# Kernel optimization log

Hardware: AMD Instinct MI355X
Metric: run time of the kernel (lower is better)

## Reference

```python
import jax, jax.numpy as jnp
import numpy as np

D_MODEL = 1024
N_HEADS = 16
HEAD_DIM = D_MODEL // N_HEADS  # 64
D_LATENT = 4 * (D_MODEL // 4)  # 1024
LN_EPS = 1e-5
NORM_EPS = 1e-12


def setup_inputs() -> dict:
    key = jax.random.key(0)
    ks = jax.random.split(key, 20)
    B, S = 2, 2048
    s = lambda fan_in: 1.0 / np.sqrt(fan_in)
    inp = {
        "query": jax.random.normal(ks[0], (B, S, D_MODEL), jnp.float32),
        "key_in": jax.random.normal(ks[1], (B, S, D_MODEL), jnp.float32),
        "value": jax.random.normal(ks[2], (B, S, D_MODEL), jnp.float32),
        # z_proj
        "Wz": jax.random.uniform(ks[3], (D_MODEL, D_LATENT), jnp.float32, -s(D_MODEL), s(D_MODEL)),
        "bz": jax.random.uniform(ks[4], (D_LATENT,), jnp.float32, -s(D_MODEL), s(D_MODEL)),
        # z_norm (LayerNorm)
        "ln_g": jnp.ones((D_LATENT,), jnp.float32),
        "ln_b": jnp.zeros((D_LATENT,), jnp.float32),
        # q/r/h projections: d_latent -> n_heads*head_dim
        "Wq": jax.random.uniform(ks[5], (D_LATENT, N_HEADS * HEAD_DIM), jnp.float32, -s(D_LATENT), s(D_LATENT)),
        "bq": jax.random.uniform(ks[6], (N_HEADS * HEAD_DIM,), jnp.float32, -s(D_LATENT), s(D_LATENT)),
        "Wr": jax.random.uniform(ks[7], (D_LATENT, N_HEADS * HEAD_DIM), jnp.float32, -s(D_LATENT), s(D_LATENT)),
        "br": jax.random.uniform(ks[8], (N_HEADS * HEAD_DIM,), jnp.float32, -s(D_LATENT), s(D_LATENT)),
        "Wh": jax.random.uniform(ks[9], (D_LATENT, N_HEADS * HEAD_DIM), jnp.float32, -s(D_LATENT), s(D_LATENT)),
        "bh": jax.random.uniform(ks[10], (N_HEADS * HEAD_DIM,), jnp.float32, -s(D_LATENT), s(D_LATENT)),
        # phi_proj: head_dim -> head_dim (shared across heads, applied to Q and R)
        "Wphi": jax.random.uniform(ks[11], (HEAD_DIM, HEAD_DIM), jnp.float32, -s(HEAD_DIM), s(HEAD_DIM)),
        "bphi": jax.random.uniform(ks[12], (HEAD_DIM,), jnp.float32, -s(HEAD_DIM), s(HEAD_DIM)),
        # out_proj
        "Wo": jax.random.uniform(ks[13], (D_MODEL, D_MODEL), jnp.float32, -s(D_MODEL), s(D_MODEL)),
        "bo": jax.random.uniform(ks[14], (D_MODEL,), jnp.float32, -s(D_MODEL), s(D_MODEL)),
    }
    return inp


def reference(query, key_in, value, Wz, bz, ln_g, ln_b, Wq, bq, Wr, br, Wh, bh, Wphi, bphi, Wo, bo):
    # NOTE: the original module ignores key_in and value entirely.
    B, S, _ = query.shape
    # latent projection + LayerNorm
    Z = query @ Wz + bz
    mu = jnp.mean(Z, axis=-1, keepdims=True)
    var = jnp.mean(jnp.square(Z - mu), axis=-1, keepdims=True)
    Z = (Z - mu) * jax.lax.rsqrt(var + LN_EPS) * ln_g + ln_b
    # Q, R, H projections -> [B, S, H, D]
    Q = (Z @ Wq + bq).reshape(B, S, N_HEADS, HEAD_DIM)
    R = (Z @ Wr + br).reshape(B, S, N_HEADS, HEAD_DIM)
    Hv = (Z @ Wh + bh).reshape(B, S, N_HEADS, HEAD_DIM)
    # phasor activation Psi(v) = v * exp(i * (v Wphi + bphi))
    phiQ = Q @ Wphi + bphi
    phiR = R @ Wphi + bphi
    # Re(Q' conj(R')) = (Q cos phiQ)(R cos phiR) + (Q sin phiQ)(R sin phiR)
    # stack real/imag components along head_dim so a single einsum gives the real part
    Qc = jnp.concatenate([Q * jnp.cos(phiQ), Q * jnp.sin(phiQ)], axis=-1)  # [B,S,H,2D]
    Rc = jnp.concatenate([R * jnp.cos(phiR), R * jnp.sin(phiR)], axis=-1)  # [B,S,H,2D]
    scores = jnp.einsum('bqhd,bkhd->bhqk', Qc, Rc)  # real part of complex QK^H
    # L2 row-normalization (torch F.normalize p=2 dim=-1, eps=1e-12)
    norm = jnp.sqrt(jnp.sum(jnp.square(scores), axis=-1, keepdims=True))
    attn = scores / jnp.maximum(norm, NORM_EPS)
    out = jnp.einsum('bhqk,bkhd->bqhd', attn, Hv).reshape(B, S, D_MODEL)
    return out @ Wo + bo
```

## Files before the change

### kernel.cpp

```cpp
#include <hip/hip_runtime.h>

#define DEV __device__ __forceinline__

typedef __bf16 bf16x8 __attribute__((ext_vector_type(8)));
typedef float f32x4 __attribute__((ext_vector_type(4)));

DEV float b2f(__bf16 v) { return (float)v; }
DEV __bf16 f2b(float v) { return (__bf16)v; }

DEV void gload16(const __bf16* g, __bf16* l) {
  __builtin_amdgcn_global_load_lds((const __attribute__((address_space(1))) unsigned*)g,
                                   (__attribute__((address_space(3))) unsigned*)l, 16, 0, 0);
}

__global__ void detect_k(const unsigned short* __restrict__ q, int* __restrict__ mode) {
  const int lane = threadIdx.x & 63;
  int cntNaN = 0, cntSmall = 0;
  for (int i = lane; i < 16384; i += 64) {
    const unsigned ef = (q[i] >> 7) & 0xFF;
    if (ef == 0xFF) cntNaN++;
    if (ef < 0x70) cntSmall++;
  }
#pragma unroll
  for (int o = 32; o > 0; o >>= 1) {
    cntNaN += __shfl_down(cntNaN, o);
    cntSmall += __shfl_down(cntSmall, o);
  }
  if (lane == 0) *mode = (cntNaN >= 4) ? 1 : ((cntSmall > 2000) ? 2 : 0);
}

__global__ __launch_bounds__(256) void qcvt_k(const void* __restrict__ src,
                                              __bf16* __restrict__ dst,
                                              int n8, const int* __restrict__ mode) {
  const int i = blockIdx.x * 256 + threadIdx.x;
  if (i >= n8) return;
  const int m = *mode;
  union { __bf16 h[8]; int4 u; } pk;
  if (m == 1) {
    const float4* p = (const float4*)src + (size_t)i * 2;
    const float4 a = p[0], b = p[1];
    pk.h[0] = f2b(a.x); pk.h[1] = f2b(a.y); pk.h[2] = f2b(a.z); pk.h[3] = f2b(a.w);
    pk.h[4] = f2b(b.x); pk.h[5] = f2b(b.y); pk.h[6] = f2b(b.z); pk.h[7] = f2b(b.w);
  } else if (m == 2) {
    const _Float16* p = (const _Float16*)src + (size_t)i * 8;
#pragma unroll
    for (int t = 0; t < 8; t++) pk.h[t] = f2b((float)p[t]);
  } else {
    pk.u = ((const int4*)src)[i];
  }
  ((int4*)dst)[i] = pk.u;
}

struct CvtJobs {
  const void* src[9];
  __bf16* dst[9];
};
__global__ __launch_bounds__(256) void cvt_all_k(CvtJobs J, const int* __restrict__ mode) {
  const int bb = blockIdx.x;
  int job, off;
  if (bb < 4) { job = bb; off = 0; }
  else if (bb == 4) { job = 4; off = 0; }
  else if (bb < 9) { job = 5; off = (bb - 5) * 1024; }
  else { job = 6 + (bb - 9); off = 0; }
  const int n = (job == 4) ? 64 : (job == 5) ? 4096 : 1024;
  const int m = *mode;
  const void* s = J.src[job];
  __bf16* d = J.dst[job];
  const int rem = n - off;
  const int cnt = rem > 1024 ? 1024 : rem;
  for (int i = threadIdx.x; i < cnt; i += 256) {
    const int idx = off + i;
    const float v = (m == 1) ? ((const float*)s)[idx]
                  : (m == 2) ? (float)((const _Float16*)s)[idx]
                             : b2f(((const __bf16*)s)[idx]);
    d[idx] = f2b(v);
  }
}

struct TJobs {
  const void* src[5];
  __bf16* dst[5];
};
__global__ __launch_bounds__(256) void tcvt_all_k(TJobs J, const int* __restrict__ mode) {
  __shared__ __bf16 tile[64][68];
  const void* in = J.src[blockIdx.z];
  __bf16* out = J.dst[blockIdx.z];
  const int c0 = blockIdx.x * 64, r0 = blockIdx.y * 64;
  const int tid = threadIdx.x;
  const int m = *mode;
  for (int i = tid; i < 64 * 16; i += 256) {
    int r = i >> 4, cc = (i & 15) * 4;
    const size_t base = (size_t)(r0 + r) * 1024 + c0 + cc;
    if (m == 1) {
      float4 v = *(const float4*)((const float*)in + base);
      tile[r][cc + 0] = f2b(v.x);
      tile[r][cc + 1] = f2b(v.y);
      tile[r][cc + 2] = f2b(v.z);
      tile[r][cc + 3] = f2b(v.w);
    } else if (m == 2) {
      const _Float16* p = (const _Float16*)in + base;
      tile[r][cc + 0] = f2b((float)p[0]);
      tile[r][cc + 1] = f2b((float)p[1]);
      tile[r][cc + 2] = f2b((float)p[2]);
      tile[r][cc + 3] = f2b((float)p[3]);
    } else {
      *(uint2*)&tile[r][cc] = *(const uint2*)((const __bf16*)in + base);
    }
  }
  __syncthreads();
  for (int i = tid; i < 64 * 16; i += 256) {
    int c = i >> 4, rr = (i & 15) * 4;
    union { __bf16 h[4]; uint2 u; } pk;
    pk.h[0] = tile[rr + 0][c];
    pk.h[1] = tile[rr + 1][c];
    pk.h[2] = tile[rr + 2][c];
    pk.h[3] = tile[rr + 3][c];
    *(uint2*)&out[(size_t)(c0 + c) * 1024 + r0 + rr] = pk.u;
  }
}

template <bool OUT_F32>
__global__ __launch_bounds__(256) void gemm2p_k(const __bf16* __restrict__ A,
                                                const __bf16* __restrict__ BT,
                                                const __bf16* __restrict__ bias,
                                                void* __restrict__ Cout,
                                                int M, int N, int K) {
  __shared__ __bf16 As[2][64 * 64];
  __shared__ __bf16 Bs[2][64 * 64];
  const int tid = threadIdx.x, lane = tid & 63, wv = tid >> 6;
  const int quad = lane >> 4, l16 = lane & 15;
  const int nblk = gridDim.x, chunk = nblk >> 3;
  const int hb = blockIdx.x;
  const int lb = (hb & 7) * chunk + (hb >> 3);
  const int mcnt = M >> 6;
  const int ni = lb / mcnt, mi = lb - ni * mcnt;
  const int m0 = mi * 64, n0 = ni * 64;
  const int wm = (wv >> 1) * 32, wn = (wv & 1) * 32;

  int s_src[2];
#pragma unroll
  for (int u = 0; u < 2; u++) {
    const int ci = tid + u * 256;
    const int r = ci >> 3, cc = ci & 7;
    s_src[u] = r * K + ((cc ^ (r & 7)) * 8);
  }

#define GSTAGE(BUF, K0)                                                   \
  {                                                                       \
    const __bf16* a_ = A + (size_t)m0 * K + (K0);                         \
    const __bf16* b_ = BT + (size_t)n0 * K + (K0);                        \
    gload16(a_ + s_src[0], &As[BUF][tid * 8]);                            \
    gload16(a_ + s_src[1], &As[BUF][(tid + 256) * 8]);                    \
    gload16(b_ + s_src[0], &Bs[BUF][tid * 8]);                            \
    gload16(b_ + s_src[1], &Bs[BUF][(tid + 256) * 8]);                    \
  }

  f32x4 acc[2][2] = {};
  const int nk = K >> 6;
  const int key = l16 & 7;

  GSTAGE(0, 0);
  __syncthreads();

  for (int t = 0; t < nk; ++t) {
    const int cur = t & 1;
    if (t + 1 < nk) GSTAGE(cur ^ 1, (t + 1) * 64);
#pragma unroll
    for (int s = 0; s < 2; s++) {
      const int co = ((4 * s + quad) ^ key) * 8;
      bf16x8 af[2], bfr[2];
#pragma unroll
      for (int i = 0; i < 2; i++) af[i] = *(const bf16x8*)&As[cur][(wm + i * 16 + l16) * 64 + co];
#pragma unroll
      for (int j = 0; j < 2; j++) bfr[j] = *(const bf16x8*)&Bs[cur][(wn + j * 16 + l16) * 64 + co];
#pragma unroll
      for (int i = 0; i < 2; i++)
#pragma unroll
        for (int j = 0; j < 2; j++)
          acc[i][j] = __builtin_amdgcn_mfma_f32_16x16x32_bf16(af[i], bfr[j], acc[i][j], 0, 0, 0);
    }
    __syncthreads();
  }
#undef GSTAGE

#pragma unroll
  for (int j = 0; j < 2; j++) {
    const int col = n0 + wn + j * 16 + l16;
    const float bv = b2f(bias[col]);
#pragma unroll
    for (int i = 0; i < 2; i++) {
#pragma unroll
      for (int r = 0; r < 4; r++) {
        const int row = m0 + wm + i * 16 + quad * 4 + r;
        const float v = acc[i][j][r] + bv;
        if (OUT_F32)
          ((float*)Cout)[(size_t)row * N + col] = v;
        else
          ((__bf16*)Cout)[(size_t)row * N + col] = f2b(v);
      }
    }
  }
}

__global__ __launch_bounds__(256) void qrh2p_k(const __bf16* __restrict__ A,
                                               const __bf16* __restrict__ BT3,
                                               const __bf16* __restrict__ bias3,
                                               __bf16* __restrict__ Qf,
                                               __bf16* __restrict__ Rf,
                                               __bf16* __restrict__ Hv,
                                               int M) {
  __shared__ __bf16 As[2][64 * 64];
  __shared__ __bf16 Bs[2][64 * 64];
  const int tid = threadIdx.x, lane = tid & 63, wv = tid >> 6;
  const int quad = lane >> 4, l16 = lane & 15;
  const int nblk = gridDim.x, chunk = nblk >> 3;
  const int hb = blockIdx.x;
  const int lb = (hb & 7) * chunk + (hb >> 3);
  const int mcnt = M >> 6;
  const int ni = lb / mcnt, mi = lb - ni * mcnt;
  const int m0 = mi * 64, n0g = ni * 64;
  const int which = n0g >> 10, n0 = n0g & 1023;
  __bf16* out = (which == 0) ? Qf : (which == 1) ? Rf : Hv;
  const int wm = (wv >> 1) * 32, wn = (wv & 1) * 32;
  const int K = 1024;

  int s_src[2];
#pragma unroll
  for (int u = 0; u < 2; u++) {
    const int ci = tid + u * 256;
    const int r = ci >> 3, cc = ci & 7;
    s_src[u] = r * K + ((cc ^ (r & 7)) * 8);
  }

#define GSTAGE(BUF, K0)                                                   \
  {                                                                       \
    const __bf16* a_ = A + (size_t)m0 * K + (K0);                         \
    const __bf16* b_ = BT3 + (size_t)n0g * K + (K0);                      \
    gload16(a_ + s_src[0], &As[BUF][tid * 8]);                            \
    gload16(a_ + s_src[1], &As[BUF][(tid + 256) * 8]);                    \
    gload16(b_ + s_src[0], &Bs[BUF][tid * 8]);                            \
    gload16(b_ + s_src[1], &Bs[BUF][(tid + 256) * 8]);                    \
  }

  f32x4 acc[2][2] = {};
  const int key = l16 & 7;

  GSTAGE(0, 0);
  __syncthreads();

  for (int t = 0; t < 16; ++t) {
    const int cur = t & 1;
    if (t + 1 < 16) GSTAGE(cur ^ 1, (t + 1) * 64);
#pragma unroll
    for (int s = 0; s < 2; s++) {
      const int co = ((4 * s + quad) ^ key) * 8;
      bf16x8 af[2], bfr[2];
#pragma unroll
      for (int i = 0; i < 2; i++) af[i] = *(const bf16x8*)&As[cur][(wm + i * 16 + l16) * 64 + co];
#pragma unroll
      for (int j = 0; j < 2; j++) bfr[j] = *(const bf16x8*)&Bs[cur][(wn + j * 16 + l16) * 64 + co];
#pragma unroll
      for (int i = 0; i < 2; i++)
#pragma unroll
        for (int j = 0; j < 2; j++)
          acc[i][j] = __builtin_amdgcn_mfma_f32_16x16x32_bf16(af[i], bfr[j], acc[i][j], 0, 0, 0);
    }
    __syncthreads();
  }
#undef GSTAGE

#pragma unroll
  for (int j = 0; j < 2; j++) {
    const int colg = n0g + wn + j * 16 + l16;
    const int col = n0 + wn + j * 16 + l16;
    const float bv = b2f(bias3[colg]);
#pragma unroll
    for (int i = 0; i < 2; i++) {
#pragma unroll
      for (int r = 0; r < 4; r++) {
        const int row = m0 + wm + i * 16 + quad * 4 + r;
        out[(size_t)row * 1024 + col] = f2b(acc[i][j][r] + bv);
      }
    }
  }
}

__global__ __launch_bounds__(256) void ln_k(const float* __restrict__ Zraw,
                                            const __bf16* __restrict__ g,
                                            const __bf16* __restrict__ bb,
                                            __bf16* __restrict__ Z) {
  __shared__ float red[8];
  const int row = blockIdx.x, tid = threadIdx.x, lane = tid & 63, wv = tid >> 6;
  const float* x = Zraw + (size_t)row * 1024;
  float4 v = *(const float4*)&x[tid * 4];
  float s = v.x + v.y + v.z + v.w;
  float ss = v.x * v.x + v.y * v.y + v.z * v.z + v.w * v.w;
#pragma unroll
  for (int o = 32; o > 0; o >>= 1) {
    s += __shfl_down(s, o);
    ss += __shfl_down(ss, o);
  }
  if (lane == 0) { red[wv] = s; red[4 + wv] = ss; }
  __syncthreads();
  const float S = red[0] + red[1] + red[2] + red[3];
  const float SS = red[4] + red[5] + red[6] + red[7];
  const float mu = S * (1.f / 1024.f);
  const float var = SS * (1.f / 1024.f) - mu * mu;
  const float rstd = rsqrtf(var + 1e-5f);
  const int c = tid * 4;
  float xs[4] = {v.x, v.y, v.z, v.w};
  union { __bf16 h[4]; uint2 u; } pk;
#pragma unroll
  for (int i = 0; i < 4; i++)
    pk.h[i] = f2b((xs[i] - mu) * rstd * b2f(g[c + i]) + b2f(bb[c + i]));
  *(uint2*)&Z[(size_t)row * 1024 + c] = pk.u;
}

__global__ __launch_bounds__(256) void phasor_mfma_k(const __bf16* __restrict__ Qf,
                                                     const __bf16* __restrict__ Rf,
                                                     const __bf16* __restrict__ Wphi,
                                                     const __bf16* __restrict__ bphi,
                                                     __bf16* __restrict__ Qc,
                                                     __bf16* __restrict__ Rc) {
  __shared__ __bf16 Qs[128][76];
  __shared__ __bf16 WT[64][76];
  const __bf16* in = blockIdx.y ? Rf : Qf;
  __bf16* out = blockIdx.y ? Rc : Qc;
  const int tid = threadIdx.x, lane = tid & 63, wv = tid >> 6;
  const int quad = lane >> 4, l16 = lane & 15;
  const size_t m0 = (size_t)blockIdx.x * 128;
  for (int i = tid; i < 1024; i += 256) {
    int r = i >> 3, c = (i & 7) * 8;
    *(int4*)&Qs[r][c] = *(const int4*)&in[(m0 + r) * 64 + c];
  }
  for (int i = tid; i < 4096; i += 256) WT[i & 63][i >> 6] = Wphi[i];
  __syncthreads();
  f32x4 acc[2][4] = {};
#pragma unroll
  for (int s = 0; s < 2; s++) {
    const int ka = s * 32 + quad * 8;
    bf16x8 bfr[4];
#pragma unroll
    for (int j = 0; j < 4; j++) bfr[j] = *(const bf16x8*)&WT[j * 16 + l16][ka];
#pragma unroll
    for (int i = 0; i < 2; i++) {
      const bf16x8 af = *(const bf16x8*)&Qs[wv * 32 + i * 16 + l16][ka];
#pragma unroll
      for (int j = 0; j < 4; j++)
        acc[i][j] = __builtin_amdgcn_mfma_f32_16x16x32_bf16(af, bfr[j], acc[i][j], 0, 0, 0);
    }
  }
#pragma unroll
  for (int i = 0; i < 2; i++)
#pragma unroll
    for (int j = 0; j < 4; j++) {
      const int col = j * 16 + l16;
      const float bj = b2f(bphi[col]);
#pragma unroll
      for (int r = 0; r < 4; r++) {
        const int row = wv * 32 + i * 16 + quad * 4 + r;
        const float phi = acc[i][j][r] + bj;
        float sn, cs;
        __sincosf(phi, &sn, &cs);
        const float qv = b2f(Qs[row][col]);
        const size_t ob = (m0 + row) * 128;
        out[ob + col] = f2b(qv * cs);
        out[ob + 64 + col] = f2b(qv * sn);
      }
    }
}

__global__ __launch_bounds__(256) void hvt_k(const __bf16* __restrict__ Hv,
                                             __bf16* __restrict__ HvT, int S) {
  __shared__ __bf16 t[64][72];
  const int tt = blockIdx.x * 64, h = blockIdx.y, b = blockIdx.z;
  const int tid = threadIdx.x;
  for (int i = tid; i < 512; i += 256) {
    int tok = i >> 3, dc = (i & 7) * 8;
    *(int4*)&t[tok][dc] = *(const int4*)&Hv[((size_t)(b * S + tt + tok) * 16 + h) * 64 + dc];
  }
  __syncthreads();
  for (int i = tid; i < 1024; i += 256) {
    int d = i >> 4, tc = (i & 15) * 4;
    union { __bf16 h4[4]; uint2 u; } pk;
    pk.h4[0] = t[tc + 0][d];
    pk.h4[1] = t[tc + 1][d];
    pk.h4[2] = t[tc + 2][d];
    pk.h4[3] = t[tc + 3][d];
    *(uint2*)&HvT[(((size_t)(b * 16 + h) * 64 + d) * S) + tt + tc] = pk.u;
  }
}

__global__ __launch_bounds__(256) void attn_k(const __bf16* __restrict__ Qc,
                                              const __bf16* __restrict__ Rc,
                                              const __bf16* __restrict__ HvT,
                                              __bf16* __restrict__ Aout, int S) {
  __shared__ __bf16 Rs[2][64 * 128];
  __shared__ __bf16 Hs[2][64 * 64];
  const int tid = threadIdx.x, lane = tid & 63, wv = tid >> 6;
  const int quad = lane >> 4, l16 = lane & 15;
  const int nblk = gridDim.x;
  const int chunk = nblk >> 3;
  const int hb = blockIdx.x;
  const int lb = (hb & 7) * chunk + (hb >> 3);
  const int nx = nblk >> 5;
  const int x = lb % nx;
  const int rest = lb / nx;
  const int h = rest & 15, b = rest >> 4;
  const int q0 = x * 64;

  bf16x8 qf[4];
  {
    const __bf16* qp = Qc + ((size_t)(b * S + q0 + wv * 16 + l16) * 16 + h) * 128 + quad * 8;
#pragma unroll
    for (int s = 0; s < 4; s++) qf[s] = *(const bf16x8*)(qp + s * 32);
  }

  const size_t rcb = ((size_t)b * S * 16 + h) * 128;
  const size_t hvb = (size_t)(b * 16 + h) * 64 * S;

  int rs_src[4], hs_src[2];
#pragma unroll
  for (int u = 0; u < 4; u++) {
    const int r = 4 * (wv * 4 + u) + (lane >> 4);
    rs_src[u] = r * 2048 + (((lane & 15) ^ (r & 7)) * 8);
  }
#pragma unroll
  for (int u = 0; u < 2; u++) {
    const int row = 8 * (wv * 2 + u) + (lane >> 3);
    hs_src[u] = row * S + (((lane & 7) ^ (row & 7)) * 8);
  }

#define STAGE(BUF, TILE)                                                        \
  {                                                                             \
    const __bf16* rc_ = Rc + rcb + (size_t)(TILE) * 64 * 2048;                  \
    const __bf16* hv_ = HvT + hvb + (TILE) * 64;                                \
    _Pragma("unroll")                                                           \
    for (int u = 0; u < 4; u++)                                                 \
      gload16(rc_ + rs_src[u], &Rs[BUF][(wv * 4 + u) * 512]);                   \
    _Pragma("unroll")                                                           \
    for (int u = 0; u < 2; u++)                                                 \
      gload16(hv_ + hs_src[u], &Hs[BUF][(wv * 2 + u) * 512]);                   \
  }

  f32x4 oacc[4] = {};
  float rssq = 0.f;
  const int nt = S >> 6;

  STAGE(0, 0);
  __syncthreads();

  const int srcA = ((quad & 1) << 1) | (quad >> 1);
  const int adA = ((srcA << 4) | l16) << 2;
  const int adB = (((srcA ^ 1) << 4) | l16) << 2;
  const bool par = (quad & 1) != 0;
  const bool hi = (quad >> 1) != 0;
  const int key = l16 & 7;

  for (int it = 0; it < nt; ++it) {
    const int cur = it & 1;
    if (it + 1 < nt) STAGE(cur ^ 1, it + 1);

    f32x4 sacc[4] = {};
    __builtin_amdgcn_s_setprio(1);
#pragma unroll
    for (int s = 0; s < 4; s++) {
      const int co = ((4 * s + quad) ^ key) * 8;
#pragma unroll
      for (int jt = 0; jt < 4; jt++) {
        const bf16x8 rf = *(const bf16x8*)&Rs[cur][(jt * 16 + l16) * 128 + co];
        sacc[jt] = __builtin_amdgcn_mfma_f32_16x16x32_bf16(rf, qf[s], sacc[jt], 0, 0, 0);
      }
    }
    __builtin_amdgcn_s_setprio(0);

    unsigned pk[4][2];
#pragma unroll
    for (int jt = 0; jt < 4; jt++) {
      rssq += sacc[jt][0] * sacc[jt][0] + sacc[jt][1] * sacc[jt][1] +
              sacc[jt][2] * sacc[jt][2] + sacc[jt][3] * sacc[jt][3];
      union { __bf16 h2[2]; unsigned u; } p0, p1;
      p0.h2[0] = f2b(sacc[jt][0]); p0.h2[1] = f2b(sacc[jt][1]);
      p1.h2[0] = f2b(sacc[jt][2]); p1.h2[1] = f2b(sacc[jt][3]);
      pk[jt][0] = p0.u; pk[jt][1] = p1.u;
    }

#pragma unroll
    for (int s2 = 0; s2 < 2; s2++) {
      bf16x8 hf[4];
      const int co2 = ((4 * s2 + quad) ^ key) * 8;
#pragma unroll
      for (int jd = 0; jd < 4; jd++)
        hf[jd] = *(const bf16x8*)&Hs[cur][(jd * 16 + l16) * 64 + co2];
      const int jA = 2 * s2, jB = 2 * s2 + 1;
      const unsigned o0 = par ? pk[jB][0] : pk[jA][0];
      const unsigned o1 = par ? pk[jB][1] : pk[jA][1];
      const unsigned o2 = par ? pk[jA][0] : pk[jB][0];
      const unsigned o3 = par ? pk[jA][1] : pk[jB][1];
      const unsigned r0 = (unsigned)__builtin_amdgcn_ds_bpermute(adA, (int)o0);
      const unsigned r1 = (unsigned)__builtin_amdgcn_ds_bpermute(adA, (int)o1);
      const unsigned r2 = (unsigned)__builtin_amdgcn_ds_bpermute(adB, (int)o2);
      const unsigned r3 = (unsigned)__builtin_amdgcn_ds_bpermute(adB, (int)o3);
      union { unsigned u[4]; bf16x8 v; } bw;
      bw.u[0] = hi ? r2 : r0;
      bw.u[1] = hi ? r3 : r1;
      bw.u[2] = hi ? r0 : r2;
      bw.u[3] = hi ? r1 : r3;
      __builtin_amdgcn_s_setprio(1);
#pragma unroll
      for (int jd = 0; jd < 4; jd++)
        oacc[jd] = __builtin_amdgcn_mfma_f32_16x16x32_bf16(hf[jd], bw.v, oacc[jd], 0, 0, 0);
      __builtin_amdgcn_s_setprio(0);
    }
    __syncthreads();
  }
#undef STAGE

  {
    float t = rssq;
    t += __shfl_xor(t, 16);
    t += __shfl_xor(t, 32);
    const float inv = 1.0f / fmaxf(sqrtf(t), 1e-12f);
    const size_t orow = (size_t)(b * S + q0 + wv * 16 + l16) * 1024 + h * 64;
#pragma unroll
    for (int jd = 0; jd < 4; jd++) {
      union { __bf16 h4[4]; uint2 u2; } o;
#pragma unroll
      for (int r = 0; r < 4; r++) o.h4[r] = f2b(oacc[jd][r] * inv);
      *(uint2*)&Aout[orow + jd * 16 + quad * 4] = o.u2;
    }
  }
}

extern "C" void kernel_launch(void* const* d_in, const int* in_sizes, int n_in,
                              void* d_out, int out_size, void* d_ws, size_t ws_size,
                              hipStream_t stream) {
  const void* query = d_in[0];
  const void* Wz = d_in[3];
  const void* bz = d_in[4];
  const void* ln_g = d_in[5];
  const void* ln_b = d_in[6];
  const void* Wq = d_in[7];
  const void* bq = d_in[8];
  const void* Wr = d_in[9];
  const void* br = d_in[10];
  const void* Wh = d_in[11];
  const void* bh = d_in[12];
  const void* Wphi = d_in[13];
  const void* bphi = d_in[14];
  const void* Wo = d_in[15];
  const void* bo = d_in[16];

  const int n_q = in_sizes[0];
  const int Srows = n_q >> 10;
  const int S = Srows >> 1;

  char* ws = (char*)d_ws;
  const size_t MB = 1024 * 1024;

  int* mode = (int*)(ws);
  __bf16* sv = (__bf16*)(ws + 4096);
  __bf16* bz_c   = sv + 0 * 4096;
  __bf16* lng_c  = sv + 1 * 4096;
  __bf16* lnb_c  = sv + 2 * 4096;
  __bf16* bo_c   = sv + 3 * 4096;
  __bf16* bphi_c = sv + 4 * 4096;
  __bf16* wphi_c = sv + 5 * 4096;
  __bf16* bqrh   = sv + 6 * 4096;
  __bf16* WzT    = (__bf16*)(ws + 1 * MB);
  __bf16* WoT    = (__bf16*)(ws + 3 * MB);
  __bf16* WqrhT  = (__bf16*)(ws + 5 * MB);
  float*  Zraw   = (float*) (ws + 11 * MB);
  __bf16* Z      = (__bf16*)(ws + 27 * MB);
  __bf16* Qf     = (__bf16*)(ws + 35 * MB);
  __bf16* Rf     = (__bf16*)(ws + 43 * MB);
  __bf16* Hv     = (__bf16*)(ws + 51 * MB);
  __bf16* Qbf    = (__bf16*)(ws + 59 * MB);
  __bf16* Rc     = (__bf16*)(ws + 59 * MB);
  __bf16* Qc     = (__bf16*)(ws + 11 * MB);
  __bf16* HvT    = (__bf16*)(ws + 27 * MB);
  __bf16* Aout   = (__bf16*)(ws + 35 * MB);

  dim3 blk(256);
  detect_k<<<1, 64, 0, stream>>>((const unsigned short*)query, mode);

  CvtJobs cj;
  cj.src[0] = bz;   cj.dst[0] = bz_c;
  cj.src[1] = ln_g; cj.dst[1] = lng_c;
  cj.src[2] = ln_b; cj.dst[2] = lnb_c;
  cj.src[3] = bo;   cj.dst[3] = bo_c;
  cj.src[4] = bphi; cj.dst[4] = bphi_c;
  cj.src[5] = Wphi; cj.dst[5] = wphi_c;
  cj.src[6] = bq;   cj.dst[6] = bqrh;
  cj.src[7] = br;   cj.dst[7] = bqrh + 1024;
  cj.src[8] = bh;   cj.dst[8] = bqrh + 2048;
  cvt_all_k<<<12, blk, 0, stream>>>(cj, mode);

  TJobs tj;
  tj.src[0] = Wz; tj.dst[0] = WzT;
  tj.src[1] = Wo; tj.dst[1] = WoT;
  tj.src[2] = Wq; tj.dst[2] = WqrhT;
  tj.src[3] = Wr; tj.dst[3] = WqrhT + 1024 * 1024;
  tj.src[4] = Wh; tj.dst[4] = WqrhT + 2 * 1024 * 1024;
  tcvt_all_k<<<dim3(16, 16, 5), blk, 0, stream>>>(tj, mode);

  qcvt_k<<<(Srows * 1024 / 8 + 255) / 256, blk, 0, stream>>>(query, Qbf, Srows * 128, mode);

  const int mcnt = Srows / 64;
  gemm2p_k<true><<<16 * mcnt, blk, 0, stream>>>(Qbf, WzT, bz_c, (void*)Zraw,
                                                Srows, 1024, 1024);
  ln_k<<<Srows, blk, 0, stream>>>(Zraw, lng_c, lnb_c, Z);
  qrh2p_k<<<48 * mcnt, blk, 0, stream>>>(Z, WqrhT, bqrh, Qf, Rf, Hv, Srows);
  phasor_mfma_k<<<dim3((Srows * 16) / 128, 2), blk, 0, stream>>>(Qf, Rf, wphi_c, bphi_c, Qc, Rc);
  hvt_k<<<dim3(S / 64, 16, 2), blk, 0, stream>>>(Hv, HvT, S);
  attn_k<<<dim3((S / 64) * 32), blk, 0, stream>>>(Qc, Rc, HvT, Aout, S);
  gemm2p_k<true><<<16 * mcnt, blk, 0, stream>>>(Aout, WoT, bo_c, d_out,
                                                Srows, 1024, 1024);
}
```

Before: 371.0 us.

## Double output tile sizes in QRH projection and attention kernels for more reuse

The QRH projection GEMM now computes 64x128 tiles, with each wave owning a 32x64 sub-tile, so its grid is halved. The attention kernel now processes 128 query rows per block, 32 per wave, so each staged R/Hv tile in shared memory feeds twice as many MFMAs. The aim is to cut global and LDS traffic per FLOP and amortize barriers. The cost is more accumulator registers, which may reduce occupancy, and fewer blocks: 512 attention blocks on a 256-CU part. The setprio hints around the MFMA loops were also dropped.

```diff
diff --git a/kernel.cpp b/kernel.cpp
--- a/kernel.cpp
+++ b/kernel.cpp
@@ -210,7 +210,7 @@
                                                __bf16* __restrict__ Hv,
                                                int M) {
   __shared__ __bf16 As[2][64 * 64];
-  __shared__ __bf16 Bs[2][64 * 64];
+  __shared__ __bf16 Bs[2][128 * 64];
   const int tid = threadIdx.x, lane = tid & 63, wv = tid >> 6;
   const int quad = lane >> 4, l16 = lane & 15;
   const int nblk = gridDim.x, chunk = nblk >> 3;
@@ -218,15 +218,15 @@
   const int lb = (hb & 7) * chunk + (hb >> 3);
   const int mcnt = M >> 6;
   const int ni = lb / mcnt, mi = lb - ni * mcnt;
-  const int m0 = mi * 64, n0g = ni * 64;
+  const int m0 = mi * 64, n0g = ni * 128;
   const int which = n0g >> 10, n0 = n0g & 1023;
   __bf16* out = (which == 0) ? Qf : (which == 1) ? Rf : Hv;
-  const int wm = (wv >> 1) * 32, wn = (wv & 1) * 32;
+  const int wm = (wv >> 1) * 32, wn = (wv & 1) * 64;
   const int K = 1024;
 
-  int s_src[2];
-#pragma unroll
-  for (int u = 0; u < 2; u++) {
+  int s_src[4];
+#pragma unroll
+  for (int u = 0; u < 4; u++) {
     const int ci = tid + u * 256;
     const int r = ci >> 3, cc = ci & 7;
     s_src[u] = r * K + ((cc ^ (r & 7)) * 8);
@@ -238,11 +238,12 @@
     const __bf16* b_ = BT3 + (size_t)n0g * K + (K0);                      \
     gload16(a_ + s_src[0], &As[BUF][tid * 8]);                            \
     gload16(a_ + s_src[1], &As[BUF][(tid + 256) * 8]);                    \
-    gload16(b_ + s_src[0], &Bs[BUF][tid * 8]);                            \
-    gload16(b_ + s_src[1], &Bs[BUF][(tid + 256) * 8]);                    \
-  }
-
-  f32x4 acc[2][2] = {};
+    _Pragma("unroll")                                                     \
+    for (int u = 0; u < 4; u++)                                           \
+      gload16(b_ + s_src[u], &Bs[BUF][(tid + u * 256) * 8]);              \
+  }
+
+  f32x4 acc[2][4] = {};
   const int key = l16 & 7;
 
   GSTAGE(0, 0);
@@ -254,15 +255,15 @@
 #pragma unroll
     for (int s = 0; s < 2; s++) {
       const int co = ((4 * s + quad) ^ key) * 8;
-      bf16x8 af[2], bfr[2];
+      bf16x8 af[2], bfr[4];
 #pragma unroll
       for (int i = 0; i < 2; i++) af[i] = *(const bf16x8*)&As[cur][(wm + i * 16 + l16) * 64 + co];
 #pragma unroll
-      for (int j = 0; j < 2; j++) bfr[j] = *(const bf16x8*)&Bs[cur][(wn + j * 16 + l16) * 64 + co];
+      for (int j = 0; j < 4; j++) bfr[j] = *(const bf16x8*)&Bs[cur][(wn + j * 16 + l16) * 64 + co];
 #pragma unroll
       for (int i = 0; i < 2; i++)
 #pragma unroll
-        for (int j = 0; j < 2; j++)
+        for (int j = 0; j < 4; j++)
           acc[i][j] = __builtin_amdgcn_mfma_f32_16x16x32_bf16(af[i], bfr[j], acc[i][j], 0, 0, 0);
     }
     __syncthreads();
@@ -270,7 +271,7 @@
 #undef GSTAGE
 
 #pragma unroll
-  for (int j = 0; j < 2; j++) {
+  for (int j = 0; j < 4; j++) {
     const int colg = n0g + wn + j * 16 + l16;
     const int col = n0 + wn + j * 16 + l16;
     const float bv = b2f(bias3[colg]);
@@ -407,13 +408,14 @@
   const int x = lb % nx;
   const int rest = lb / nx;
   const int h = rest & 15, b = rest >> 4;
-  const int q0 = x * 64;
-
-  bf16x8 qf[4];
-  {
-    const __bf16* qp = Qc + ((size_t)(b * S + q0 + wv * 16 + l16) * 16 + h) * 128 + quad * 8;
-#pragma unroll
-    for (int s = 0; s < 4; s++) qf[s] = *(const bf16x8*)(qp + s * 32);
+  const int q0 = x * 128;
+
+  bf16x8 qf[2][4];
+#pragma unroll
+  for (int i = 0; i < 2; i++) {
+    const __bf16* qp = Qc + ((size_t)(b * S + q0 + wv * 32 + i * 16 + l16) * 16 + h) * 128 + quad * 8;
+#pragma unroll
+    for (int s = 0; s < 4; s++) qf[i][s] = *(const bf16x8*)(qp + s * 32);
   }
 
   const size_t rcb = ((size_t)b * S * 16 + h) * 128;
@@ -443,8 +445,8 @@
       gload16(hv_ + hs_src[u], &Hs[BUF][(wv * 2 + u) * 512]);                   \
   }
 
-  f32x4 oacc[4] = {};
-  float rssq = 0.f;
+  f32x4 oacc[2][4] = {};
+  float rssq[2] = {};
   const int nt = S >> 6;
 
   STAGE(0, 0);
@@ -461,29 +463,31 @@
     const int cur = it & 1;
     if (it + 1 < nt) STAGE(cur ^ 1, it + 1);
 
-    f32x4 sacc[4] = {};
-    __builtin_amdgcn_s_setprio(1);
+    f32x4 sacc[4][2] = {};
 #pragma unroll
     for (int s = 0; s < 4; s++) {
       const int co = ((4 * s + quad) ^ key) * 8;
 #pragma unroll
       for (int jt = 0; jt < 4; jt++) {
         const bf16x8 rf = *(const bf16x8*)&Rs[cur][(jt * 16 + l16) * 128 + co];
-        sacc[jt] = __builtin_amdgcn_mfma_f32_16x16x32_bf16(rf, qf[s], sacc[jt], 0, 0, 0);
+#pragma unroll
+        for (int i = 0; i < 2; i++)
+          sacc[jt][i] = __builtin_amdgcn_mfma_f32_16x16x32_bf16(rf, qf[i][s], sacc[jt][i], 0, 0, 0);
       }
     }
-    __builtin_amdgcn_s_setprio(0);
-
-    unsigned pk[4][2];
-#pragma unroll
-    for (int jt = 0; jt < 4; jt++) {
-      rssq += sacc[jt][0] * sacc[jt][0] + sacc[jt][1] * sacc[jt][1] +
-              sacc[jt][2] * sacc[jt][2] + sacc[jt][3] * sacc[jt][3];
-      union { __bf16 h2[2]; unsigned u; } p0, p1;
-      p0.h2[0] = f2b(sacc[jt][0]); p0.h2[1] = f2b(sacc[jt][1]);
-      p1.h2[0] = f2b(sacc[jt][2]); p1.h2[1] = f2b(sacc[jt][3]);
-      pk[jt][0] = p0.u; pk[jt][1] = p1.u;
-    }
+
+    unsigned pk[4][2][2];
+#pragma unroll
+    for (int jt = 0; jt < 4; jt++)
+#pragma unroll
+      for (int i = 0; i < 2; i++) {
+        rssq[i] += sacc[jt][i][0] * sacc[jt][i][0] + sacc[jt][i][1] * sacc[jt][i][1] +
+                   sacc[jt][i][2] * sacc[jt][i][2] + sacc[jt][i][3] * sacc[jt][i][3];
+        union { __bf16 h2[2]; unsigned u; } p0, p1;
+        p0.h2[0] = f2b(sacc[jt][i][0]); p0.h2[1] = f2b(sacc[jt][i][1]);
+        p1.h2[0] = f2b(sacc[jt][i][2]); p1.h2[1] = f2b(sacc[jt][i][3]);
+        pk[jt][i][0] = p0.u; pk[jt][i][1] = p1.u;
+      }
 
 #pragma unroll
     for (int s2 = 0; s2 < 2; s2++) {
@@ -493,40 +497,42 @@
       for (int jd = 0; jd < 4; jd++)
         hf[jd] = *(const bf16x8*)&Hs[cur][(jd * 16 + l16) * 64 + co2];
       const int jA = 2 * s2, jB = 2 * s2 + 1;
-      const unsigned o0 = par ? pk[jB][0] : pk[jA][0];
-      const unsigned o1 = par ? pk[jB][1] : pk[jA][1];
-      const unsigned o2 = par ? pk[jA][0] : pk[jB][0];
-      const unsigned o3 = par ? pk[jA][1] : pk[jB][1];
-      const unsigned r0 = (unsigned)__builtin_amdgcn_ds_bpermute(adA, (int)o0);
-      const unsigned r1 = (unsigned)__builtin_amdgcn_ds_bpermute(adA, (int)o1);
-      const unsigned r2 = (unsigned)__builtin_amdgcn_ds_bpermute(adB, (int)o2);
-      const unsigned r3 = (unsigned)__builtin_amdgcn_ds_bpermute(adB, (int)o3);
-      union { unsigned u[4]; bf16x8 v; } bw;
-      bw.u[0] = hi ? r2 : r0;
-      bw.u[1] = hi ? r3 : r1;
-      bw.u[2] = hi ? r0 : r2;
-      bw.u[3] = hi ? r1 : r3;
-      __builtin_amdgcn_s_setprio(1);
-#pragma unroll
-      for (int jd = 0; jd < 4; jd++)
-        oacc[jd] = __builtin_amdgcn_mfma_f32_16x16x32_bf16(hf[jd], bw.v, oacc[jd], 0, 0, 0);
-      __builtin_amdgcn_s_setprio(0);
+#pragma unroll
+      for (int i = 0; i < 2; i++) {
+        const unsigned o0 = par ? pk[jB][i][0] : pk[jA][i][0];
+        const unsigned o1 = par ? pk[jB][i][1] : pk[jA][i][1];
+        const unsigned o2 = par ? pk[jA][i][0] : pk[jB][i][0];
+        const unsigned o3 = par ? pk[jA][i][1] : pk[jB][i][1];
+        const unsigned r0 = (unsigned)__builtin_amdgcn_ds_bpermute(adA, (int)o0);
+        const unsigned r1 = (unsigned)__builtin_amdgcn_ds_bpermute(adA, (int)o1);
+        const unsigned r2 = (unsigned)__builtin_amdgcn_ds_bpermute(adB, (int)o2);
+        const unsigned r3 = (unsigned)__builtin_amdgcn_ds_bpermute(adB, (int)o3);
+        union { unsigned u[4]; bf16x8 v; } bw;
+        bw.u[0] = hi ? r2 : r0;
+        bw.u[1] = hi ? r3 : r1;
+        bw.u[2] = hi ? r0 : r2;
+        bw.u[3] = hi ? r1 : r3;
+#pragma unroll
+        for (int jd = 0; jd < 4; jd++)
+          oacc[i][jd] = __builtin_amdgcn_mfma_f32_16x16x32_bf16(hf[jd], bw.v, oacc[i][jd], 0, 0, 0);
+      }
     }
     __syncthreads();
   }
 #undef STAGE
 
-  {
-    float t = rssq;
+#pragma unroll
+  for (int i = 0; i < 2; i++) {
+    float t = rssq[i];
     t += __shfl_xor(t, 16);
     t += __shfl_xor(t, 32);
     const float inv = 1.0f / fmaxf(sqrtf(t), 1e-12f);
-    const size_t orow = (size_t)(b * S + q0 + wv * 16 + l16) * 1024 + h * 64;
+    const size_t orow = (size_t)(b * S + q0 + wv * 32 + i * 16 + l16) * 1024 + h * 64;
 #pragma unroll
     for (int jd = 0; jd < 4; jd++) {
       union { __bf16 h4[4]; uint2 u2; } o;
 #pragma unroll
-      for (int r = 0; r < 4; r++) o.h4[r] = f2b(oacc[jd][r] * inv);
+      for (int r = 0; r < 4; r++) o.h4[r] = f2b(oacc[i][jd][r] * inv);
       *(uint2*)&Aout[orow + jd * 16 + quad * 4] = o.u2;
     }
   }
@@ -610,10 +616,10 @@
   gemm2p_k<true><<<16 * mcnt, blk, 0, stream>>>(Qbf, WzT, bz_c, (void*)Zraw,
                                                 Srows, 1024, 1024);
   ln_k<<<Srows, blk, 0, stream>>>(Zraw, lng_c, lnb_c, Z);
-  qrh2p_k<<<48 * mcnt, blk, 0, stream>>>(Z, WqrhT, bqrh, Qf, Rf, Hv, Srows);
+  qrh2p_k<<<24 * mcnt, blk, 0, stream>>>(Z, WqrhT, bqrh, Qf, Rf, Hv, Srows);
   phasor_mfma_k<<<dim3((Srows * 16) / 128, 2), blk, 0, stream>>>(Qf, Rf, wphi_c, bphi_c, Qc, Rc);
   hvt_k<<<dim3(S / 64, 16, 2), blk, 0, stream>>>(Hv, HvT, S);
-  attn_k<<<dim3((S / 64) * 32), blk, 0, stream>>>(Qc, Rc, HvT, Aout, S);
+  attn_k<<<dim3((S / 128) * 32), blk, 0, stream>>>(Qc, Rc, HvT, Aout, S);
   gemm2p_k<true><<<16 * mcnt, blk, 0, stream>>>(Aout, WoT, bo_c, d_out,
                                                 Srows, 1024, 1024);
 }
```

New measurement: 311.4 us. -16.0%, faster.
